# Optimization experiments

Measured on AMD Instinct MI355X. Metric: run time of the kernel, lower is better.

The kernel has to match this reference:

```python
import jax, jax.numpy as jnp
import numpy as np

B, T, L = 64, 256, 20
WV, WD = 100000, 300
CV, CD = 100, 100
PV, PD = 50, 100
NF, K = 100, 3
H = 256
D0 = WD + PD + NF        # 500, layer-0 LSTM input
D1 = 2 * H               # 512, later layers' input


def _lstm_dir(gx, mask, w_hh, reverse):
    # gx: [B,T,4H] precomputed input contribution + bias; mask: [B,T,1]
    if reverse:
        gx = gx[:, ::-1]
        mask = mask[:, ::-1]
    b, h = gx.shape[0], w_hh.shape[1]
    h0 = jnp.zeros((b, h), gx.dtype)

    def step(carry, xs):
        hp, cp = carry
        g_t, m_t = xs
        gates = g_t + hp @ w_hh.T
        i, f, g, o = jnp.split(gates, 4, axis=-1)
        i = jax.nn.sigmoid(i); f = jax.nn.sigmoid(f)
        o = jax.nn.sigmoid(o); g = jnp.tanh(g)
        c_new = f * cp + i * g
        h_new = o * jnp.tanh(c_new)
        hn = m_t * h_new + (1.0 - m_t) * hp   # masked step (pad positions keep state)
        cn = m_t * c_new + (1.0 - m_t) * cp
        return (hn, cn), hn

    _, hs = jax.lax.scan(step, (h0, h0), (gx.transpose(1, 0, 2), mask.transpose(1, 0, 2)))
    hs = hs.transpose(1, 0, 2)
    return hs[:, ::-1] if reverse else hs


def _bilstm_layer(x, mask, w_ih, w_hh, b):
    # w_ih: [2,4H,D], w_hh: [2,4H,H], b: [2,4H] (b_ih+b_hh combined)
    outs = []
    for d in range(2):
        gx = jnp.einsum('btd,gd->btg', x, w_ih[d]) + b[d]
        outs.append(_lstm_dir(gx, mask, w_hh[d], reverse=(d == 1)))
    return jnp.concatenate(outs, axis=-1)


def setup_inputs() -> dict:
    key = jax.random.key(0)
    ks = jax.random.split(key, 16)
    s = 0.05
    inp = {
        'input_word': jax.random.randint(ks[0], (B, T), 0, WV),
        'input_char': jax.random.randint(ks[1], (B, T, L), 0, CV),
        'input_pos': jax.random.randint(ks[2], (B, T), 0, PV),
        'mask': jnp.ones((B, T), jnp.float32),
        'emb_word': jax.random.normal(ks[3], (WV, WD), jnp.float32) * s,
        'emb_char': jax.random.normal(ks[4], (CV, CD), jnp.float32) * s,
        'emb_pos': jax.random.normal(ks[5], (PV, PD), jnp.float32) * s,
        'conv_w': jax.random.normal(ks[6], (NF, CD, K), jnp.float32) * s,
        'conv_b': jax.random.normal(ks[7], (NF,), jnp.float32) * s,
        'w_ih0': jax.random.normal(ks[8], (2, 4 * H, D0), jnp.float32) * s,
        'w_hh0': jax.random.normal(ks[9], (2, 4 * H, H), jnp.float32) * s,
        'b0': jax.random.normal(ks[10], (2, 4 * H), jnp.float32) * s,
        'w_ih1': jax.random.normal(ks[11], (2, 4 * H, D1), jnp.float32) * s,
        'w_hh1': jax.random.normal(ks[12], (2, 4 * H, H), jnp.float32) * s,
        'b1': jax.random.normal(ks[13], (2, 4 * H), jnp.float32) * s,
        'w_ih2': jax.random.normal(ks[14], (2, 4 * H, D1), jnp.float32) * s,
        'w_hh2': jax.random.normal(ks[15], (2, 4 * H, H), jnp.float32) * s,
        'b2': jax.random.normal(jax.random.fold_in(key, 99), (2, 4 * H), jnp.float32) * s,
    }
    return inp


def reference(input_word, input_char, input_pos, mask,
              emb_word, emb_char, emb_pos, conv_w, conv_b,
              w_ih0, w_hh0, b0, w_ih1, w_hh1, b1, w_ih2, w_hh2, b2):
    # dropout layers are identity in eval mode
    word = emb_word[input_word]                       # [B,T,WD]
    b, t, l = input_char.shape
    ch = emb_char[input_char].reshape(b * t, l, CD).transpose(0, 2, 1)  # [BT,CD,L]
    conv = jax.lax.conv_general_dilated(
        ch, conv_w, window_strides=(1,), padding=[(K - 1, K - 1)],
        dimension_numbers=('NCH', 'OIH', 'NCH')) + conv_b[None, :, None]
    ch = jnp.tanh(conv.max(axis=2)).reshape(b, t, NF)  # [B,T,NF]
    pos = emb_pos[input_pos]                           # [B,T,PD]
    x = jnp.concatenate([word, ch, pos], axis=-1)      # [B,T,D0]
    m = mask[..., None]
    x = _bilstm_layer(x, m, w_ih0, w_hh0, b0)
    x = _bilstm_layer(x, m, w_ih1, w_hh1, b1)
    x = _bilstm_layer(x, m, w_ih2, w_hh2, b2)
    return x                                           # [B,T,2H]
```

## Files before the change

kernel.cpp:

```cpp
#include <hip/hip_runtime.h>
#include <cstdint>
#include <cstddef>
#include <type_traits>
#include <utility>

typedef unsigned short u16;
typedef short short8 __attribute__((ext_vector_type(8)));
typedef __bf16 bf16x8 __attribute__((ext_vector_type(8)));
typedef float float4v __attribute__((ext_vector_type(4)));

__device__ __forceinline__ float bf2f(u16 u) {
  union { uint32_t i; float f; } v; v.i = ((uint32_t)u) << 16; return v.f;
}
__device__ __forceinline__ u16 f2bf(float f) {
  union { uint32_t i; float f; } v; v.f = f;
  uint32_t u = v.i;
  return (u16)((u + 0x7FFFu + ((u >> 16) & 1u)) >> 16);
}

__device__ __forceinline__ float fsig(float x) {
  float e = __expf(-x);
  return __builtin_amdgcn_rcpf(1.0f + e);
}
__device__ __forceinline__ float ftanh(float x) {
  float e = __expf(2.0f * x);
  return 1.0f - 2.0f * __builtin_amdgcn_rcpf(e + 1.0f);
}

template <class V, class = void> struct MfmaTakesShort : std::false_type {};
template <class V>
struct MfmaTakesShort<V, std::void_t<decltype(__builtin_amdgcn_mfma_f32_16x16x32_bf16(
    std::declval<V>(), std::declval<V>(), std::declval<float4v>(), 0, 0, 0))>>
    : std::true_type {};

template <bool UseShort> struct MF {
  template <class V>
  static __device__ __forceinline__ float4v run(V a, V b, float4v c) {
    return __builtin_amdgcn_mfma_f32_16x16x32_bf16(a, b, c, 0, 0, 0);
  }
};
template <> struct MF<false> {
  template <class V>
  static __device__ __forceinline__ float4v run(V a, V b, float4v c) {
    return __builtin_amdgcn_mfma_f32_16x16x32_bf16(
        __builtin_bit_cast(bf16x8, a), __builtin_bit_cast(bf16x8, b), c, 0, 0, 0);
  }
};
__device__ __forceinline__ float4v mfma_bf16(short8 a, short8 b, float4v c) {
  return MF<MfmaTakesShort<short8>::value>::run(a, b, c);
}

__global__ void k_cvt_wih(const float* __restrict__ w, u16* __restrict__ o, int Kin) {
  int id = blockIdx.x * 256 + threadIdx.x;
  int n = id >> 9, k = id & 511;
  o[id] = (k < Kin) ? f2bf(w[(long)n * Kin + k]) : (u16)0;
}

__global__ void k_cvt_whh(const float* __restrict__ w, u16* __restrict__ o) {
  int id = blockIdx.x * 256 + threadIdx.x;
  o[id] = f2bf(w[id]);
}

__global__ void k_proj(const float* __restrict__ ec, const float* __restrict__ cw,
                       u16* __restrict__ proj) {
  int v = blockIdx.x, idx = threadIdx.x;
  if (idx >= 300) return;
  int k = idx / 100, nf = idx % 100;
  float s = 0.f;
  for (int cd = 0; cd < 100; cd++)
    s += ec[v * 100 + cd] * cw[(nf * 100 + cd) * 3 + k];
  proj[v * 300 + k * 100 + nf] = f2bf(s);
}

__global__ void k_embed(const int* __restrict__ iw, const int* __restrict__ ip,
                        const float* __restrict__ ew, const float* __restrict__ ep,
                        u16* __restrict__ x) {
  int row = blockIdx.x, j = threadIdx.x;
  u16 v;
  if (j < 300) v = f2bf(ew[(long)iw[row] * 300 + j]);
  else if (j < 400) return;
  else if (j < 500) v = f2bf(ep[ip[row] * 100 + (j - 400)]);
  else v = 0;
  x[row * 512 + j] = v;
}

__global__ __launch_bounds__(128) void k_charconv(const int* __restrict__ ic,
                                                  const u16* __restrict__ proj,
                                                  const float* __restrict__ cb,
                                                  u16* __restrict__ x) {
  __shared__ u16 pl[30000];
  __shared__ int ids[20];
  int tid = threadIdx.x;
  for (int i = tid; i < 15000; i += 128)
    ((uint32_t*)pl)[i] = ((const uint32_t*)proj)[i];
  float bias = (tid < 100) ? cb[tid] : 0.f;
  for (int r = 0; r < 16; r++) {
    int row = blockIdx.x * 16 + r;
    __syncthreads();
    if (tid < 20) ids[tid] = ic[row * 20 + tid];
    __syncthreads();
    if (tid < 100) {
      float mx = -1e30f;
      for (int p = 0; p < 22; p++) {
        float s = 0.f;
#pragma unroll
        for (int k = 0; k < 3; k++) {
          int q = p + k - 2;
          if (q >= 0 && q < 20) s += bf2f(pl[ids[q] * 300 + k * 100 + tid]);
        }
        mx = fmaxf(mx, s);
      }
      x[row * 512 + 300 + tid] = f2bf(ftanh(mx + bias));
    }
  }
}

template <bool GXF32>
__global__ __launch_bounds__(256) void k_gemm(const u16* __restrict__ A,
                                              const u16* __restrict__ Bm,
                                              const float* __restrict__ bias,
                                              void* __restrict__ Cv) {
  __shared__ u16 lA[128 * 64];
  __shared__ u16 lB[128 * 64];
  int tid = threadIdx.x;
  int w = tid >> 6, l = tid & 63, q = l >> 4, c16 = l & 15;
  int wm = w >> 1, wn = w & 1;
  int m0 = blockIdx.y * 128, n0 = blockIdx.x * 128;
  float4v acc[4][4];
#pragma unroll
  for (int i = 0; i < 4; i++)
#pragma unroll
    for (int j = 0; j < 4; j++) acc[i][j] = (float4v){0.f, 0.f, 0.f, 0.f};

  for (int kk = 0; kk < 512; kk += 64) {
    __syncthreads();
#pragma unroll
    for (int j = 0; j < 4; j++) {
      int idx = j * 256 + tid;
      int m = idx >> 3, k8 = (idx & 7) * 8;
      *(short8*)(lA + idx * 8) = *(const short8*)(A + (long)(m0 + m) * 512 + kk + k8);
      *(short8*)(lB + idx * 8) = *(const short8*)(Bm + (long)(n0 + m) * 512 + kk + k8);
    }
    __syncthreads();
#pragma unroll
    for (int kt = 0; kt < 2; kt++) {
      short8 af[4], bfv[4];
#pragma unroll
      for (int mt = 0; mt < 4; mt++)
        af[mt] = *(const short8*)(lA + (wm * 64 + mt * 16 + c16) * 64 + kt * 32 + q * 8);
#pragma unroll
      for (int nt = 0; nt < 4; nt++)
        bfv[nt] = *(const short8*)(lB + (wn * 64 + nt * 16 + c16) * 64 + kt * 32 + q * 8);
#pragma unroll
      for (int mt = 0; mt < 4; mt++)
#pragma unroll
        for (int nt = 0; nt < 4; nt++)
          acc[mt][nt] = mfma_bf16(af[mt], bfv[nt], acc[mt][nt]);
    }
  }
#pragma unroll
  for (int mt = 0; mt < 4; mt++)
#pragma unroll
    for (int nt = 0; nt < 4; nt++) {
      int ng = n0 + wn * 64 + nt * 16 + c16;
      float bv = bias[ng];
#pragma unroll
      for (int r = 0; r < 4; r++) {
        long mg = m0 + wm * 64 + mt * 16 + q * 4 + r;
        float val = acc[mt][nt][r] + bv;
        if constexpr (GXF32) ((float*)Cv)[mg * 2048 + ng] = val;
        else ((u16*)Cv)[mg * 2048 + ng] = f2bf(val);
      }
    }
}

template <bool GXF32, bool OUTF32>
__global__ __launch_bounds__(512, 2) void k_recur(
    const void* __restrict__ gxv, const u16* __restrict__ whh,
    const float* __restrict__ mask, void* __restrict__ outv,
    unsigned long long* __restrict__ hx, unsigned* __restrict__ flags) {
  __shared__ u16 hls[2][16 * 136];
  int tid = threadIdx.x;
  int w = tid >> 6, l = tid & 63;
  int row = l & 15;
  int cg = l >> 4;
  int c4 = cg * 4;
  int blk = blockIdx.x;
  int pair = blk & 7, half = blk >> 3;
  int bg = pair >> 1, d = pair & 1;
  int b0 = bg * 16;
  int ht = half * 8 + w;
  const u16* Wd = whh + d * (1024 * 256);

  for (int i = tid; i < 16 * 136; i += 512) hls[0][i] = 0;

  short8 Breg[32];
#pragma unroll
  for (int g = 0; g < 4; g++)
#pragma unroll
    for (int j = 0; j < 8; j++) {
      int ktg = (j < 4) ? (half * 4 + j) : ((half ^ 1) * 4 + (j - 4));
      Breg[g * 8 + j] =
          *(const short8*)(Wd + ((g * 16 + ht) * 16 + row) * 256 + ktg * 32 + cg * 8);
    }

  float c_[4] = {0.f, 0.f, 0.f, 0.f};
  unsigned long long hp64 = 0ull;
  __syncthreads();

  const float* gxf = (const float*)gxv;
  const u16* gxh = (const u16*)gxv;
  float* outf = (float*)outv;
  u16* outh = (u16*)outv;

  int grow = b0 + row;
  const float* mrowp = mask + grow * 256;
  size_t gxbase = (size_t)grow * 524288 + d * 1024 + ht * 16 + c4;
  long obase = ((long)grow * 256) * 512 + d * 256 + ht * 16 + c4;

  using GxT = std::conditional_t<GXF32, float4v, unsigned long long>;
  GxT gxc[4], gxn[4];
  float mcur, mnxt;

  {
    int t0 = d ? 255 : 0;
    mcur = mrowp[t0];
#pragma unroll
    for (int g = 0; g < 4; g++) {
      if constexpr (GXF32)
        gxc[g] = *(const float4v*)(gxf + gxbase + (size_t)t0 * 2048 + g * 256);
      else
        gxc[g] = *(const unsigned long long*)(gxh + gxbase + (size_t)t0 * 2048 + g * 256);
    }
  }

#pragma unroll 1
  for (int s = 0; s < 256; s++) {
    int t = d ? (255 - s) : s;
    const u16* hrd = hls[s & 1];
    u16* hwr = hls[(s & 1) ^ 1];

    short8 png[4];
    if (s > 0) {
      unsigned fidx = (unsigned)((s - 1) * 16 + pair * 2 + (half ^ 1));
      unsigned cnt = 0;
      while (__hip_atomic_load(&flags[fidx], __ATOMIC_RELAXED,
                               __HIP_MEMORY_SCOPE_AGENT) == 0u) {
        if (++cnt > 1000000u) break;
        __builtin_amdgcn_s_sleep(1);
      }
      const unsigned long long* ps =
          hx + ((size_t)(pair * 2 + ((s - 1) & 1)) * 2 + (half ^ 1)) * 512;
#pragma unroll
      for (int ktl = 0; ktl < 4; ktl++) {
        unsigned long long v0 = __hip_atomic_load(
            &ps[(ktl * 8 + cg * 2 + 0) * 16 + row], __ATOMIC_RELAXED,
            __HIP_MEMORY_SCOPE_AGENT);
        unsigned long long v1 = __hip_atomic_load(
            &ps[(ktl * 8 + cg * 2 + 1) * 16 + row], __ATOMIC_RELAXED,
            __HIP_MEMORY_SCOPE_AGENT);
        union { unsigned long long u[2]; short8 s8; } uu;
        uu.u[0] = v0; uu.u[1] = v1;
        png[ktl] = uu.s8;
      }
    }
    __builtin_amdgcn_sched_barrier(0);

    float4v acc[4];
#pragma unroll
    for (int g = 0; g < 4; g++) acc[g] = (float4v){0.f, 0.f, 0.f, 0.f};
#pragma unroll
    for (int ktl = 0; ktl < 4; ktl++) {
      short8 b = *(const short8*)(hrd + row * 136 + ktl * 32 + cg * 8);
#pragma unroll
      for (int g = 0; g < 4; g++)
        acc[g] = mfma_bf16(Breg[g * 8 + ktl], b, acc[g]);
    }
    if (s > 0) {
#pragma unroll
      for (int ktl = 0; ktl < 4; ktl++)
#pragma unroll
        for (int g = 0; g < 4; g++)
          acc[g] = mfma_bf16(Breg[g * 8 + 4 + ktl], png[ktl], acc[g]);
    }

    float mt = mcur, mo = 1.f - mcur;
    float hnv[4];
    unsigned long long hn64 = 0ull;
#pragma unroll
    for (int r = 0; r < 4; r++) {
      float gi, gf, gg, go;
      if constexpr (GXF32) {
        gi = gxc[0][r]; gf = gxc[1][r]; gg = gxc[2][r]; go = gxc[3][r];
      } else {
        gi = bf2f((u16)(gxc[0] >> (r * 16)));
        gf = bf2f((u16)(gxc[1] >> (r * 16)));
        gg = bf2f((u16)(gxc[2] >> (r * 16)));
        go = bf2f((u16)(gxc[3] >> (r * 16)));
      }
      float iv = fsig(acc[0][r] + gi);
      float fv = fsig(acc[1][r] + gf);
      float gv = ftanh(acc[2][r] + gg);
      float ov = fsig(acc[3][r] + go);
      float hpo = bf2f((u16)(hp64 >> (r * 16)));
      float cn = fv * c_[r] + iv * gv;
      float hn = ov * ftanh(cn);
      hn = mt * hn + mo * hpo;
      cn = mt * cn + mo * c_[r];
      c_[r] = cn;
      hnv[r] = hn;
      hn64 |= ((unsigned long long)f2bf(hn)) << (r * 16);
    }

    if (s < 255) {
      __hip_atomic_store(
          &hx[((size_t)(pair * 2 + (s & 1)) * 2 + half) * 512 + (w * 4 + cg) * 16 + row],
          hn64, __ATOMIC_RELAXED, __HIP_MEMORY_SCOPE_AGENT);
      __builtin_amdgcn_sched_barrier(0);
      *(unsigned long long*)(hwr + row * 136 + w * 16 + c4) = hn64;
      if constexpr (OUTF32) {
        float4v ov4 = {hnv[0], hnv[1], hnv[2], hnv[3]};
        *(float4v*)(outf + obase + (long)t * 512) = ov4;
      } else {
        *(unsigned long long*)(outh + obase + (long)t * 512) = hn64;
      }
      int tn = d ? (254 - s) : (s + 1);
      mnxt = mrowp[tn];
#pragma unroll
      for (int g = 0; g < 4; g++) {
        if constexpr (GXF32)
          gxn[g] = *(const float4v*)(gxf + gxbase + (size_t)tn * 2048 + g * 256);
        else
          gxn[g] = *(const unsigned long long*)(gxh + gxbase + (size_t)tn * 2048 + g * 256);
      }
      __builtin_amdgcn_sched_barrier(0);
      asm volatile("s_waitcnt vmcnt(6) lgkmcnt(0)" ::: "memory");
      __builtin_amdgcn_s_barrier();
      __builtin_amdgcn_sched_barrier(0);
      if (tid == 0)
        __hip_atomic_store(&flags[s * 16 + pair * 2 + half], 1u, __ATOMIC_RELAXED,
                           __HIP_MEMORY_SCOPE_AGENT);
#pragma unroll
      for (int g = 0; g < 4; g++) gxc[g] = gxn[g];
      mcur = mnxt;
    } else {
      if constexpr (OUTF32) {
        float4v ov4 = {hnv[0], hnv[1], hnv[2], hnv[3]};
        *(float4v*)(outf + obase + (long)t * 512) = ov4;
      } else {
        *(unsigned long long*)(outh + obase + (long)t * 512) = hn64;
      }
    }
    hp64 = hn64;
  }
}

extern "C" void kernel_launch(void* const* d_in, const int* in_sizes, int n_in,
                              void* d_out, int out_size, void* d_ws, size_t ws_size,
                              hipStream_t stream) {
  const int* iw = (const int*)d_in[0];
  const int* ic = (const int*)d_in[1];
  const int* ip = (const int*)d_in[2];
  const float* mask = (const float*)d_in[3];
  const float* ew = (const float*)d_in[4];
  const float* ec = (const float*)d_in[5];
  const float* ep = (const float*)d_in[6];
  const float* cw = (const float*)d_in[7];
  const float* cb = (const float*)d_in[8];
  const float* wih[3] = {(const float*)d_in[9], (const float*)d_in[12], (const float*)d_in[15]};
  const float* whh[3] = {(const float*)d_in[10], (const float*)d_in[13], (const float*)d_in[16]};
  const float* bs[3] = {(const float*)d_in[11], (const float*)d_in[14], (const float*)d_in[17]};

  char* ws = (char*)d_ws;
  size_t szX0 = (size_t)16384 * 512 * 2;
  size_t szGXf = (size_t)16384 * 2048 * 4;
  size_t szWIH = (size_t)2048 * 512 * 2;
  size_t szWHH = (size_t)2 * 1024 * 256 * 2;
  size_t szPROJ = 60032;
  size_t szHX = (size_t)8 * 2 * 2 * 4096;
  size_t szFLG = (size_t)256 * 16 * 4;
  bool f32gx = ws_size >= szX0 + szGXf + szWIH + szWHH + szPROJ + szHX + szFLG;

  size_t off = 0;
  u16* X0 = (u16*)(ws + off); off += szX0;
  void* GX = (void*)(ws + off); off += f32gx ? szGXf : (szGXf / 2);
  u16* WIHB = (u16*)(ws + off); off += szWIH;
  u16* WHHB = (u16*)(ws + off); off += szWHH;
  u16* PROJ = (u16*)(ws + off); off += szPROJ;
  unsigned long long* HX = (unsigned long long*)(ws + off); off += szHX;
  unsigned* FLG = (unsigned*)(ws + off);
  u16* X1 = (u16*)d_out;

  hipLaunchKernelGGL(k_proj, dim3(100), dim3(320), 0, stream, ec, cw, PROJ);
  hipLaunchKernelGGL(k_embed, dim3(16384), dim3(512), 0, stream, iw, ip, ew, ep, X0);
  hipLaunchKernelGGL(k_charconv, dim3(1024), dim3(128), 0, stream, ic, PROJ, cb, X0);

  const u16* Xin[3] = {X0, X1, X0};
  void* Xout[3] = {(void*)X1, (void*)X0, d_out};
  int Kin[3] = {500, 512, 512};

  for (int lyr = 0; lyr < 3; lyr++) {
    hipLaunchKernelGGL(k_cvt_wih, dim3(4096), dim3(256), 0, stream, wih[lyr], WIHB, Kin[lyr]);
    hipLaunchKernelGGL(k_cvt_whh, dim3(2048), dim3(256), 0, stream, whh[lyr], WHHB);
    hipMemsetAsync(FLG, 0, szFLG, stream);
    if (f32gx) {
      hipLaunchKernelGGL((k_gemm<true>), dim3(16, 128), dim3(256), 0, stream,
                         Xin[lyr], WIHB, bs[lyr], GX);
      if (lyr < 2)
        hipLaunchKernelGGL((k_recur<true, false>), dim3(16), dim3(512), 0, stream,
                           GX, WHHB, mask, Xout[lyr], HX, FLG);
      else
        hipLaunchKernelGGL((k_recur<true, true>), dim3(16), dim3(512), 0, stream,
                           GX, WHHB, mask, Xout[lyr], HX, FLG);
    } else {
      hipLaunchKernelGGL((k_gemm<false>), dim3(16, 128), dim3(256), 0, stream,
                         Xin[lyr], WIHB, bs[lyr], GX);
      if (lyr < 2)
        hipLaunchKernelGGL((k_recur<false, false>), dim3(16), dim3(512), 0, stream,
                           GX, WHHB, mask, Xout[lyr], HX, FLG);
      else
        hipLaunchKernelGGL((k_recur<false, true>), dim3(16), dim3(512), 0, stream,
                           GX, WHHB, mask, Xout[lyr], HX, FLG);
    }
  }
}
```

Before: 2.642 ms.

## Use per-wave flags and plain volatile exchange when paired blocks share an XCD

At startup each recurrent block records its XCC id and checks whether its partner block landed on the same XCD. If so, the cross-block hidden-state exchange and flag signalling use plain volatile loads and stores instead of agent-scope atomics. Flags move from one per block to one per wave, so each wave signals as soon as its own store is done rather than after the block barrier; consumers poll all eight with a wave-wide check. The goal is lower per-step synchronisation latency across 256 serial steps. The cost is a startup handshake, a larger flag area, and reliance on same-XCD cache coherence for volatile accesses.

```diff
diff --git a/kernel.cpp b/kernel.cpp
--- a/kernel.cpp
+++ b/kernel.cpp
@@ -25,6 +25,17 @@
 __device__ __forceinline__ float ftanh(float x) {
   float e = __expf(2.0f * x);
   return 1.0f - 2.0f * __builtin_amdgcn_rcpf(e + 1.0f);
+}
+
+__device__ __forceinline__ unsigned long long ld_u64x(
+    const unsigned long long* p, bool fastp) {
+  return fastp ? *(volatile const unsigned long long*)p
+               : __hip_atomic_load(p, __ATOMIC_RELAXED, __HIP_MEMORY_SCOPE_AGENT);
+}
+__device__ __forceinline__ void st_u64x(unsigned long long* p,
+                                        unsigned long long v, bool fastp) {
+  if (fastp) *(volatile unsigned long long*)p = v;
+  else __hip_atomic_store(p, v, __ATOMIC_RELAXED, __HIP_MEMORY_SCOPE_AGENT);
 }
 
 template <class V, class = void> struct MfmaTakesShort : std::false_type {};
@@ -180,6 +191,7 @@
     const float* __restrict__ mask, void* __restrict__ outv,
     unsigned long long* __restrict__ hx, unsigned* __restrict__ flags) {
   __shared__ u16 hls[2][16 * 136];
+  __shared__ int sFast;
   int tid = threadIdx.x;
   int w = tid >> 6, l = tid & 63;
   int row = l & 15;
@@ -192,6 +204,23 @@
   int ht = half * 8 + w;
   const u16* Wd = whh + d * (1024 * 256);
 
+  if (tid == 0) {
+    unsigned myx;
+    asm volatile("s_getreg_b32 %0, hwreg(HW_REG_XCC_ID)" : "=s"(myx));
+    int* xcds = (int*)(flags + 32768);
+    __hip_atomic_store(&xcds[blk], (int)((myx & 0xFFu) | 0x100u),
+                       __ATOMIC_RELEASE, __HIP_MEMORY_SCOPE_AGENT);
+    int pblk = pair | ((half ^ 1) << 3);
+    int pv = 0;
+    unsigned cnt = 0;
+    while ((( pv = __hip_atomic_load(&xcds[pblk], __ATOMIC_ACQUIRE,
+                                     __HIP_MEMORY_SCOPE_AGENT)) & 0x100) == 0) {
+      if (++cnt > 4000000u) break;
+      __builtin_amdgcn_s_sleep(1);
+    }
+    sFast = ((pv & 0x100) != 0 && (unsigned)(pv & 0xFF) == (myx & 0xFFu)) ? 1 : 0;
+  }
+
   for (int i = tid; i < 16 * 136; i += 512) hls[0][i] = 0;
 
   short8 Breg[32];
@@ -207,6 +236,7 @@
   float c_[4] = {0.f, 0.f, 0.f, 0.f};
   unsigned long long hp64 = 0ull;
   __syncthreads();
+  const bool fastp = (sFast != 0);
 
   const float* gxf = (const float*)gxv;
   const u16* gxh = (const u16*)gxv;
@@ -242,23 +272,27 @@
 
     short8 png[4];
     if (s > 0) {
-      unsigned fidx = (unsigned)((s - 1) * 16 + pair * 2 + (half ^ 1));
+      const unsigned* pf =
+          flags + (unsigned)((s - 1) * 16 + pair * 2 + (half ^ 1)) * 8;
       unsigned cnt = 0;
-      while (__hip_atomic_load(&flags[fidx], __ATOMIC_RELAXED,
-                               __HIP_MEMORY_SCOPE_AGENT) == 0u) {
+      for (;;) {
+        unsigned fv = fastp
+                          ? *(volatile const unsigned*)(pf + (l & 7))
+                          : __hip_atomic_load(pf + (l & 7), __ATOMIC_ACQUIRE,
+                                              __HIP_MEMORY_SCOPE_AGENT);
+        if (__all(fv != 0u)) break;
         if (++cnt > 1000000u) break;
         __builtin_amdgcn_s_sleep(1);
       }
+      __builtin_amdgcn_sched_barrier(0);
       const unsigned long long* ps =
           hx + ((size_t)(pair * 2 + ((s - 1) & 1)) * 2 + (half ^ 1)) * 512;
 #pragma unroll
       for (int ktl = 0; ktl < 4; ktl++) {
-        unsigned long long v0 = __hip_atomic_load(
-            &ps[(ktl * 8 + cg * 2 + 0) * 16 + row], __ATOMIC_RELAXED,
-            __HIP_MEMORY_SCOPE_AGENT);
-        unsigned long long v1 = __hip_atomic_load(
-            &ps[(ktl * 8 + cg * 2 + 1) * 16 + row], __ATOMIC_RELAXED,
-            __HIP_MEMORY_SCOPE_AGENT);
+        unsigned long long v0 =
+            ld_u64x(&ps[(ktl * 8 + cg * 2 + 0) * 16 + row], fastp);
+        unsigned long long v1 =
+            ld_u64x(&ps[(ktl * 8 + cg * 2 + 1) * 16 + row], fastp);
         union { unsigned long long u[2]; short8 s8; } uu;
         uu.u[0] = v0; uu.u[1] = v1;
         png[ktl] = uu.s8;
@@ -313,9 +347,9 @@
     }
 
     if (s < 255) {
-      __hip_atomic_store(
-          &hx[((size_t)(pair * 2 + (s & 1)) * 2 + half) * 512 + (w * 4 + cg) * 16 + row],
-          hn64, __ATOMIC_RELAXED, __HIP_MEMORY_SCOPE_AGENT);
+      st_u64x(&hx[((size_t)(pair * 2 + (s & 1)) * 2 + half) * 512 +
+                  (w * 4 + cg) * 16 + row],
+              hn64, fastp);
       __builtin_amdgcn_sched_barrier(0);
       *(unsigned long long*)(hwr + row * 136 + w * 16 + c4) = hn64;
       if constexpr (OUTF32) {
@@ -335,11 +369,14 @@
       }
       __builtin_amdgcn_sched_barrier(0);
       asm volatile("s_waitcnt vmcnt(6) lgkmcnt(0)" ::: "memory");
+      if (l == 0) {
+        unsigned* fp = flags + (unsigned)(s * 16 + pair * 2 + half) * 8 + w;
+        if (fastp) *(volatile unsigned*)fp = 1u;
+        else __hip_atomic_store(fp, 1u, __ATOMIC_RELEASE, __HIP_MEMORY_SCOPE_AGENT);
+      }
+      __builtin_amdgcn_sched_barrier(0);
       __builtin_amdgcn_s_barrier();
       __builtin_amdgcn_sched_barrier(0);
-      if (tid == 0)
-        __hip_atomic_store(&flags[s * 16 + pair * 2 + half], 1u, __ATOMIC_RELAXED,
-                           __HIP_MEMORY_SCOPE_AGENT);
 #pragma unroll
       for (int g = 0; g < 4; g++) gxc[g] = gxn[g];
       mcur = mnxt;
@@ -378,7 +415,7 @@
   size_t szWHH = (size_t)2 * 1024 * 256 * 2;
   size_t szPROJ = 60032;
   size_t szHX = (size_t)8 * 2 * 2 * 4096;
-  size_t szFLG = (size_t)256 * 16 * 4;
+  size_t szFLG = (size_t)(32768 + 16) * 4;
   bool f32gx = ws_size >= szX0 + szGXf + szWIH + szWHH + szPROJ + szHX + szFLG;
 
   size_t off = 0;
```

After: 4.509 ms. 1.71x slower.

## Replace flag-based handoff with sentinel-valued hidden-state exchange buffers

Applied to the files above, without the earlier changes.

Drops the separate per-step flag array. Each half-block now polls the partner's hidden-state slots directly until no slot holds an all-ones sentinel. The exchange buffer grows to four rotating slots per pair; consumers reset slots to the sentinel after use, and the buffer is memset to 0xFF per layer. The initial loads are issued before the local-half MFMAs, so the cross-block round trip overlaps with local compute, and the global store drain wait before the barrier is removed. This risks correctness if a bf16-packed hidden value ever equals the sentinel or slot reuse races; the ring depth of four is meant to prevent the latter.

```diff
diff --git a/kernel.cpp b/kernel.cpp
--- a/kernel.cpp
+++ b/kernel.cpp
@@ -178,7 +178,7 @@
 __global__ __launch_bounds__(512, 2) void k_recur(
     const void* __restrict__ gxv, const u16* __restrict__ whh,
     const float* __restrict__ mask, void* __restrict__ outv,
-    unsigned long long* __restrict__ hx, unsigned* __restrict__ flags) {
+    unsigned long long* __restrict__ hx) {
   __shared__ u16 hls[2][16 * 136];
   int tid = threadIdx.x;
   int w = tid >> 6, l = tid & 63;
@@ -191,6 +191,7 @@
   int b0 = bg * 16;
   int ht = half * 8 + w;
   const u16* Wd = whh + d * (1024 * 256);
+  constexpr unsigned long long SEN = ~0ull;
 
   for (int i = tid; i < 16 * 136; i += 512) hls[0][i] = 0;
 
@@ -240,29 +241,19 @@
     const u16* hrd = hls[s & 1];
     u16* hwr = hls[(s & 1) ^ 1];
 
-    short8 png[4];
+    unsigned long long pv0 = 0, pv1 = 0, pv2 = 0, pv3 = 0,
+                       pv4 = 0, pv5 = 0, pv6 = 0, pv7 = 0;
+    const unsigned long long* ps = nullptr;
     if (s > 0) {
-      unsigned fidx = (unsigned)((s - 1) * 16 + pair * 2 + (half ^ 1));
-      unsigned cnt = 0;
-      while (__hip_atomic_load(&flags[fidx], __ATOMIC_RELAXED,
-                               __HIP_MEMORY_SCOPE_AGENT) == 0u) {
-        if (++cnt > 1000000u) break;
-        __builtin_amdgcn_s_sleep(1);
-      }
-      const unsigned long long* ps =
-          hx + ((size_t)(pair * 2 + ((s - 1) & 1)) * 2 + (half ^ 1)) * 512;
-#pragma unroll
-      for (int ktl = 0; ktl < 4; ktl++) {
-        unsigned long long v0 = __hip_atomic_load(
-            &ps[(ktl * 8 + cg * 2 + 0) * 16 + row], __ATOMIC_RELAXED,
-            __HIP_MEMORY_SCOPE_AGENT);
-        unsigned long long v1 = __hip_atomic_load(
-            &ps[(ktl * 8 + cg * 2 + 1) * 16 + row], __ATOMIC_RELAXED,
-            __HIP_MEMORY_SCOPE_AGENT);
-        union { unsigned long long u[2]; short8 s8; } uu;
-        uu.u[0] = v0; uu.u[1] = v1;
-        png[ktl] = uu.s8;
-      }
+      ps = hx + ((size_t)(((s - 1) & 3) * 8 + pair) * 2 + (half ^ 1)) * 512;
+      pv0 = __hip_atomic_load(&ps[(0 * 8 + cg * 2 + 0) * 16 + row], __ATOMIC_RELAXED, __HIP_MEMORY_SCOPE_AGENT);
+      pv1 = __hip_atomic_load(&ps[(0 * 8 + cg * 2 + 1) * 16 + row], __ATOMIC_RELAXED, __HIP_MEMORY_SCOPE_AGENT);
+      pv2 = __hip_atomic_load(&ps[(1 * 8 + cg * 2 + 0) * 16 + row], __ATOMIC_RELAXED, __HIP_MEMORY_SCOPE_AGENT);
+      pv3 = __hip_atomic_load(&ps[(1 * 8 + cg * 2 + 1) * 16 + row], __ATOMIC_RELAXED, __HIP_MEMORY_SCOPE_AGENT);
+      pv4 = __hip_atomic_load(&ps[(2 * 8 + cg * 2 + 0) * 16 + row], __ATOMIC_RELAXED, __HIP_MEMORY_SCOPE_AGENT);
+      pv5 = __hip_atomic_load(&ps[(2 * 8 + cg * 2 + 1) * 16 + row], __ATOMIC_RELAXED, __HIP_MEMORY_SCOPE_AGENT);
+      pv6 = __hip_atomic_load(&ps[(3 * 8 + cg * 2 + 0) * 16 + row], __ATOMIC_RELAXED, __HIP_MEMORY_SCOPE_AGENT);
+      pv7 = __hip_atomic_load(&ps[(3 * 8 + cg * 2 + 1) * 16 + row], __ATOMIC_RELAXED, __HIP_MEMORY_SCOPE_AGENT);
     }
     __builtin_amdgcn_sched_barrier(0);
 
@@ -276,12 +267,36 @@
       for (int g = 0; g < 4; g++)
         acc[g] = mfma_bf16(Breg[g * 8 + ktl], b, acc[g]);
     }
+
     if (s > 0) {
-#pragma unroll
-      for (int ktl = 0; ktl < 4; ktl++)
-#pragma unroll
-        for (int g = 0; g < 4; g++)
-          acc[g] = mfma_bf16(Breg[g * 8 + 4 + ktl], png[ktl], acc[g]);
+      unsigned cnt = 0;
+      while (!__all(pv0 != SEN && pv1 != SEN && pv2 != SEN && pv3 != SEN &&
+                    pv4 != SEN && pv5 != SEN && pv6 != SEN && pv7 != SEN)) {
+        if (++cnt > 400000u) break;
+        __builtin_amdgcn_s_sleep(1);
+        pv0 = __hip_atomic_load(&ps[(0 * 8 + cg * 2 + 0) * 16 + row], __ATOMIC_RELAXED, __HIP_MEMORY_SCOPE_AGENT);
+        pv1 = __hip_atomic_load(&ps[(0 * 8 + cg * 2 + 1) * 16 + row], __ATOMIC_RELAXED, __HIP_MEMORY_SCOPE_AGENT);
+        pv2 = __hip_atomic_load(&ps[(1 * 8 + cg * 2 + 0) * 16 + row], __ATOMIC_RELAXED, __HIP_MEMORY_SCOPE_AGENT);
+        pv3 = __hip_atomic_load(&ps[(1 * 8 + cg * 2 + 1) * 16 + row], __ATOMIC_RELAXED, __HIP_MEMORY_SCOPE_AGENT);
+        pv4 = __hip_atomic_load(&ps[(2 * 8 + cg * 2 + 0) * 16 + row], __ATOMIC_RELAXED, __HIP_MEMORY_SCOPE_AGENT);
+        pv5 = __hip_atomic_load(&ps[(2 * 8 + cg * 2 + 1) * 16 + row], __ATOMIC_RELAXED, __HIP_MEMORY_SCOPE_AGENT);
+        pv6 = __hip_atomic_load(&ps[(3 * 8 + cg * 2 + 0) * 16 + row], __ATOMIC_RELAXED, __HIP_MEMORY_SCOPE_AGENT);
+        pv7 = __hip_atomic_load(&ps[(3 * 8 + cg * 2 + 1) * 16 + row], __ATOMIC_RELAXED, __HIP_MEMORY_SCOPE_AGENT);
+      }
+      union U { unsigned long long u[2]; short8 s8; };
+      U u0, u1, u2, u3;
+      u0.u[0] = pv0; u0.u[1] = pv1;
+      u1.u[0] = pv2; u1.u[1] = pv3;
+      u2.u[0] = pv4; u2.u[1] = pv5;
+      u3.u[0] = pv6; u3.u[1] = pv7;
+#pragma unroll
+      for (int g = 0; g < 4; g++) acc[g] = mfma_bf16(Breg[g * 8 + 4], u0.s8, acc[g]);
+#pragma unroll
+      for (int g = 0; g < 4; g++) acc[g] = mfma_bf16(Breg[g * 8 + 5], u1.s8, acc[g]);
+#pragma unroll
+      for (int g = 0; g < 4; g++) acc[g] = mfma_bf16(Breg[g * 8 + 6], u2.s8, acc[g]);
+#pragma unroll
+      for (int g = 0; g < 4; g++) acc[g] = mfma_bf16(Breg[g * 8 + 7], u3.s8, acc[g]);
     }
 
     float mt = mcur, mo = 1.f - mcur;
@@ -314,9 +329,8 @@
 
     if (s < 255) {
       __hip_atomic_store(
-          &hx[((size_t)(pair * 2 + (s & 1)) * 2 + half) * 512 + (w * 4 + cg) * 16 + row],
+          &hx[((size_t)((s & 3) * 8 + pair) * 2 + half) * 512 + (w * 4 + cg) * 16 + row],
           hn64, __ATOMIC_RELAXED, __HIP_MEMORY_SCOPE_AGENT);
-      __builtin_amdgcn_sched_barrier(0);
       *(unsigned long long*)(hwr + row * 136 + w * 16 + c4) = hn64;
       if constexpr (OUTF32) {
         float4v ov4 = {hnv[0], hnv[1], hnv[2], hnv[3]};
@@ -334,12 +348,14 @@
           gxn[g] = *(const unsigned long long*)(gxh + gxbase + (size_t)tn * 2048 + g * 256);
       }
       __builtin_amdgcn_sched_barrier(0);
-      asm volatile("s_waitcnt vmcnt(6) lgkmcnt(0)" ::: "memory");
+      asm volatile("s_waitcnt lgkmcnt(0)" ::: "memory");
       __builtin_amdgcn_s_barrier();
       __builtin_amdgcn_sched_barrier(0);
-      if (tid == 0)
-        __hip_atomic_store(&flags[s * 16 + pair * 2 + half], 1u, __ATOMIC_RELAXED,
-                           __HIP_MEMORY_SCOPE_AGENT);
+      if (s > 0) {
+        __hip_atomic_store(
+            &hx[((size_t)(((s - 1) & 3) * 8 + pair) * 2 + (half ^ 1)) * 512 + tid],
+            SEN, __ATOMIC_RELAXED, __HIP_MEMORY_SCOPE_AGENT);
+      }
 #pragma unroll
       for (int g = 0; g < 4; g++) gxc[g] = gxn[g];
       mcur = mnxt;
@@ -377,9 +393,8 @@
   size_t szWIH = (size_t)2048 * 512 * 2;
   size_t szWHH = (size_t)2 * 1024 * 256 * 2;
   size_t szPROJ = 60032;
-  size_t szHX = (size_t)8 * 2 * 2 * 4096;
-  size_t szFLG = (size_t)256 * 16 * 4;
-  bool f32gx = ws_size >= szX0 + szGXf + szWIH + szWHH + szPROJ + szHX + szFLG;
+  size_t szHX = (size_t)4 * 8 * 2 * 4096;
+  bool f32gx = ws_size >= szX0 + szGXf + szWIH + szWHH + szPROJ + szHX;
 
   size_t off = 0;
   u16* X0 = (u16*)(ws + off); off += szX0;
@@ -387,8 +402,7 @@
   u16* WIHB = (u16*)(ws + off); off += szWIH;
   u16* WHHB = (u16*)(ws + off); off += szWHH;
   u16* PROJ = (u16*)(ws + off); off += szPROJ;
-  unsigned long long* HX = (unsigned long long*)(ws + off); off += szHX;
-  unsigned* FLG = (unsigned*)(ws + off);
+  unsigned long long* HX = (unsigned long long*)(ws + off);
   u16* X1 = (u16*)d_out;
 
   hipLaunchKernelGGL(k_proj, dim3(100), dim3(320), 0, stream, ec, cw, PROJ);
@@ -402,25 +416,25 @@
   for (int lyr = 0; lyr < 3; lyr++) {
     hipLaunchKernelGGL(k_cvt_wih, dim3(4096), dim3(256), 0, stream, wih[lyr], WIHB, Kin[lyr]);
     hipLaunchKernelGGL(k_cvt_whh, dim3(2048), dim3(256), 0, stream, whh[lyr], WHHB);
-    hipMemsetAsync(FLG, 0, szFLG, stream);
+    hipMemsetAsync(HX, 0xFF, szHX, stream);
     if (f32gx) {
       hipLaunchKernelGGL((k_gemm<true>), dim3(16, 128), dim3(256), 0, stream,
                          Xin[lyr], WIHB, bs[lyr], GX);
       if (lyr < 2)
         hipLaunchKernelGGL((k_recur<true, false>), dim3(16), dim3(512), 0, stream,
-                           GX, WHHB, mask, Xout[lyr], HX, FLG);
+                           GX, WHHB, mask, Xout[lyr], HX);
       else
         hipLaunchKernelGGL((k_recur<true, true>), dim3(16), dim3(512), 0, stream,
-                           GX, WHHB, mask, Xout[lyr], HX, FLG);
+                           GX, WHHB, mask, Xout[lyr], HX);
     } else {
       hipLaunchKernelGGL((k_gemm<false>), dim3(16, 128), dim3(256), 0, stream,
                          Xin[lyr], WIHB, bs[lyr], GX);
       if (lyr < 2)
         hipLaunchKernelGGL((k_recur<false, false>), dim3(16), dim3(512), 0, stream,
-                           GX, WHHB, mask, Xout[lyr], HX, FLG);
+                           GX, WHHB, mask, Xout[lyr], HX);
       else
         hipLaunchKernelGGL((k_recur<false, true>), dim3(16), dim3(512), 0, stream,
-                           GX, WHHB, mask, Xout[lyr], HX, FLG);
-    }
-  }
-}
+                           GX, WHHB, mask, Xout[lyr], HX);
+    }
+  }
+}
```

New measurement: 2.319 ms. 1.14x faster.
